# Performance work log

Measured on AMD Instinct MI355X. Metric: run time of the kernel, lower is better.

The kernel has to match this reference:

```python
import jax, jax.numpy as jnp
import numpy as np

EPS = 1e-5

def _ln(v, g, b):
    m = v.mean(-1, keepdims=True)
    var = ((v - m) ** 2).mean(-1, keepdims=True)
    return (v - m) * jax.lax.rsqrt(var + EPS) * g + b

def _causal_dwconv(x, w, b):
    # x: [B,S,C], w: [C,K] depthwise kernel, b: [C]; causal (left) padding
    K = w.shape[1]
    xt = x.transpose(0, 2, 1)  # [B,C,S]
    out = jax.lax.conv_general_dilated(xt, w[:, None, :], (1,), [(K - 1, 0)],
                                       dimension_numbers=('NCH', 'OIH', 'NCH'),
                                       feature_group_count=w.shape[0])
    return out.transpose(0, 2, 1) + b

def _ssm_scan(dt, Bm, Cm, x, A):
    # dt,x: [B,S,Di]; Bm,Cm: [B,S,N]; A: [Di,N] -> y: [B,S,Di]
    def step(h, inp):
        dt_t, B_t, C_t, x_t = inp
        dA = jnp.exp(dt_t[..., None] * A)                      # [B,Di,N]
        h = dA * h + dt_t[..., None] * B_t[:, None, :] * x_t[..., None]
        return h, jnp.einsum('bdn,bn->bd', h, C_t)
    h0 = jnp.zeros((dt.shape[0], A.shape[0], A.shape[1]), dt.dtype)
    xs = (dt.swapaxes(0, 1), Bm.swapaxes(0, 1), Cm.swapaxes(0, 1), x.swapaxes(0, 1))
    _, ys = jax.lax.scan(step, h0, xs)
    return ys.swapaxes(0, 1)

def _mamba_block(u, g, b, iW, cW, cB, xW, dW, dB, Al, Dpar, oW):
    # MambaBlock: LN -> Mamba -> residual
    Di, N = Al.shape
    R = dW.shape[1]
    xn = _ln(u, g, b)
    xz = xn @ iW.T                                  # [B,S,2*Di]
    xc, z = xz[..., :Di], xz[..., Di:]
    xc = jax.nn.silu(_causal_dwconv(xc, cW, cB))
    dbl = xc @ xW.T                                 # [B,S,R+2N]
    dt = jax.nn.softplus(dbl[..., :R] @ dW.T + dB)
    Bm, Cm = dbl[..., R:R + N], dbl[..., R + N:]
    A = -jnp.exp(Al)
    y = _ssm_scan(dt, Bm, Cm, xc, A) + xc * Dpar
    y = y * jax.nn.silu(z)
    return u + y @ oW.T

def _encoder(x, ln_g, ln_b, inW, convW, convB, xprojW, dtW, dtB, A_log, Dp, outW,
             ipW, ipB, opW, opB, fln_g, fln_b):
    L = ln_g.shape[0]
    h = x
    for i in range(L):
        xp = h @ ipW[i].T + ipB[i]
        Dh = xp.shape[-1] // 2
        yf = _mamba_block(xp[..., :Dh], ln_g[i, 0], ln_b[i, 0], inW[i, 0], convW[i, 0],
                          convB[i, 0], xprojW[i, 0], dtW[i, 0], dtB[i, 0], A_log[i, 0],
                          Dp[i, 0], outW[i, 0])
        xb_rev = jnp.flip(xp[..., Dh:], axis=1)
        yb = jnp.flip(_mamba_block(xb_rev, ln_g[i, 1], ln_b[i, 1], inW[i, 1], convW[i, 1],
                                   convB[i, 1], xprojW[i, 1], dtW[i, 1], dtB[i, 1],
                                   A_log[i, 1], Dp[i, 1], outW[i, 1]), axis=1)
        h = jnp.concatenate([yf, yb], axis=-1) @ opW[i].T + opB[i]
        # dropout is identity in eval mode
    return _ln(h, fln_g, fln_b)

def setup_inputs() -> dict:
    key = jax.random.key(0)
    L, B, S, D = 2, 2, 1024, 512
    Dh, Di, N, K, R = 256, 512, 16, 4, 16
    ks = jax.random.split(key, 9)
    s = 0.02
    x = jax.random.normal(ks[0], (B, S, D), jnp.float32)
    inW = jax.random.normal(ks[1], (L, 2, 2 * Di, Dh)) * s
    convW = jax.random.normal(ks[2], (L, 2, Di, K)) * 0.2
    xprojW = jax.random.normal(ks[3], (L, 2, R + 2 * N, Di)) * s
    dtW = jax.random.normal(ks[4], (L, 2, Di, R)) * (R ** -0.5)
    u = jax.random.uniform(ks[5], (L, 2, Di))
    dt = jnp.exp(u * (np.log(0.1) - np.log(0.001)) + np.log(0.001))
    dtB = dt + jnp.log(-jnp.expm1(-dt))          # inverse softplus init
    A_log = jnp.log(jnp.broadcast_to(jnp.arange(1, N + 1, dtype=jnp.float32), (L, 2, Di, N)))
    outW = jax.random.normal(ks[6], (L, 2, Dh, Di)) * s
    ipW = jax.random.normal(ks[7], (L, D, D)) * s
    opW = jax.random.normal(ks[8], (L, D, D)) * s
    return dict(x=x, ln_g=jnp.ones((L, 2, Dh)), ln_b=jnp.zeros((L, 2, Dh)), inW=inW,
                convW=convW, convB=jnp.zeros((L, 2, Di)), xprojW=xprojW, dtW=dtW, dtB=dtB,
                A_log=A_log, Dp=jnp.ones((L, 2, Di)), outW=outW, ipW=ipW,
                ipB=jnp.zeros((L, D)), opW=opW, opB=jnp.zeros((L, D)),
                fln_g=jnp.ones((D,)), fln_b=jnp.zeros((D,)))

def reference(x, ln_g, ln_b, inW, convW, convB, xprojW, dtW, dtB, A_log, Dp, outW,
              ipW, ipB, opW, opB, fln_g, fln_b):
    return _encoder(x, ln_g, ln_b, inW, convW, convB, xprojW, dtW, dtB, A_log, Dp, outW,
                    ipW, ipB, opW, opB, fln_g, fln_b)
```

## Files before the change

### kernel.cpp

```cpp
#include <hip/hip_runtime.h>
#include <hip/hip_bf16.h>
#include <math.h>

typedef __hip_bfloat16 bf16;
typedef __attribute__((ext_vector_type(8))) short s8v;
typedef __attribute__((ext_vector_type(4))) float f4v;

#define B_ 2
#define S_ 1024
#define D_ 512
#define DH_ 256
#define DI_ 512
#define N_ 16
#define R_ 16
#define M_ 2048
#define M2_ 4096
#define T_ 16
#define CN_ 64
#define NC_ 576

#define IPW_N (2*512*512)
#define INW_N (4*1024*256)
#define OUTW_N (4*256*512)
#define OPW_N (2*512*512)

__global__ __launch_bounds__(256) void k_castall(
    const float* __restrict__ ipW, const float* __restrict__ inW,
    const float* __restrict__ outW, const float* __restrict__ opW,
    bf16* __restrict__ ipWb, bf16* __restrict__ inWb,
    bf16* __restrict__ outWb, bf16* __restrict__ opWb) {
  int i = (blockIdx.x * 256 + threadIdx.x) * 4;
  const float* s; bf16* dst; int off;
  if (i < IPW_N)                  { s = ipW;  dst = ipWb;  off = i; }
  else if (i < IPW_N + INW_N)     { s = inW;  dst = inWb;  off = i - IPW_N; }
  else if (i < IPW_N + INW_N + OUTW_N) { s = outW; dst = outWb; off = i - IPW_N - INW_N; }
  else if (i < IPW_N + INW_N + OUTW_N + OPW_N)
                                  { s = opW;  dst = opWb;  off = i - IPW_N - INW_N - OUTW_N; }
  else return;
  float4 v = *(const float4*)&s[off];
  dst[off + 0] = __float2bfloat16(v.x);
  dst[off + 1] = __float2bfloat16(v.y);
  dst[off + 2] = __float2bfloat16(v.z);
  dst[off + 3] = __float2bfloat16(v.w);
}

__global__ __launch_bounds__(256) void k_castv(const float* __restrict__ src,
                                               bf16* __restrict__ dst, int n) {
  int i = (blockIdx.x * 256 + threadIdx.x) * 4;
  if (i >= n) return;
  float4 v = *(const float4*)&src[i];
  dst[i + 0] = __float2bfloat16(v.x);
  dst[i + 1] = __float2bfloat16(v.y);
  dst[i + 2] = __float2bfloat16(v.z);
  dst[i + 3] = __float2bfloat16(v.w);
}

__global__ __launch_bounds__(256) void k_prep(const float* __restrict__ dtW,
                                              const float* __restrict__ xprojW,
                                              bf16* __restrict__ Wcomb) {
  int idx = blockIdx.x * 256 + threadIdx.x;
  if (idx >= 4 * NC_ * 512) return;
  int k = idx & 511;
  int row = (idx >> 9) % NC_;
  int wi = idx / (NC_ * 512);
  float v = 0.f;
  if (row < 512) {
    const float* dw = dtW + (size_t)wi * 512 * 16 + row * 16;
    const float* xw = xprojW + (size_t)wi * 48 * 512;
#pragma unroll
    for (int r = 0; r < 16; r++) v += dw[r] * xw[r * 512 + k];
  } else if (row < 544) {
    v = xprojW[(size_t)wi * 48 * 512 + (16 + row - 512) * 512 + k];
  }
  Wcomb[idx] = __float2bfloat16(v);
}

__global__ __launch_bounds__(256) void k_mgemm(
    const bf16* __restrict__ A, const float* __restrict__ Af,
    const bf16* __restrict__ W, long Wstr,
    const float* __restrict__ bias, int bstr,
    const float* res,
    float* C, bf16* Cb, int ldc, int K, int ep) {
  __shared__ short As[64][40];
  __shared__ short Ws[64][40];
  const int bm = blockIdx.y * 64, bn = blockIdx.x * 64;
  const int seg = bm >> 11;
  const bf16* Wp = W + (size_t)seg * Wstr;
  const float* bp = bias ? bias + (size_t)seg * bstr : nullptr;
  const int tid = threadIdx.x;
  const int wave = tid >> 6, lane = tid & 63;
  const int q = lane >> 4, l15 = lane & 15;
  const int trow = tid >> 2, tcol = (tid & 3) * 8;

  f4v acc[4];
#pragma unroll
  for (int s = 0; s < 4; s++) acc[s] = (f4v){0.f, 0.f, 0.f, 0.f};

  for (int k0 = 0; k0 < K; k0 += 32) {
    if (ep == 4) {
      int ck = k0 + tcol;
      const float* src = (ck < 256)
          ? Af + (size_t)(bm + trow) * 256 + ck
          : Af + (size_t)M_ * 256 + (size_t)((bm + trow) ^ 1023) * 256 + (ck - 256);
      float4 f0 = *(const float4*)src;
      float4 f1 = *(const float4*)(src + 4);
      float fv[8] = {f0.x, f0.y, f0.z, f0.w, f1.x, f1.y, f1.z, f1.w};
      short tmp[8];
#pragma unroll
      for (int i = 0; i < 8; i++) {
        bf16 b = __float2bfloat16(fv[i]);
        tmp[i] = *(short*)&b;
      }
      *(uint4*)&As[trow][tcol] = *(uint4*)tmp;
    } else {
      *(uint4*)&As[trow][tcol] = *(const uint4*)&A[(size_t)(bm + trow) * K + k0 + tcol];
    }
    *(uint4*)&Ws[trow][tcol] = *(const uint4*)&Wp[(size_t)(bn + trow) * K + k0 + tcol];
    __syncthreads();
    s8v bfrag = *(const s8v*)&Ws[wave * 16 + l15][q * 8];
#pragma unroll
    for (int s = 0; s < 4; s++) {
      s8v afrag = *(const s8v*)&As[s * 16 + l15][q * 8];
      acc[s] = __builtin_amdgcn_mfma_f32_16x16x32_bf16(afrag, bfrag, acc[s], 0, 0, 0);
    }
    __syncthreads();
  }
  const int col = bn + wave * 16 + l15;
#pragma unroll
  for (int s = 0; s < 4; s++) {
#pragma unroll
    for (int r = 0; r < 4; r++) {
      int row = bm + s * 16 + q * 4 + r;
      float v = acc[s][r];
      if (ep == 0) {
        if (bp) v += bp[col];
        if (res) v += res[(size_t)row * ldc + col];
        C[(size_t)row * ldc + col] = v;
      } else if (ep == 2) {
        if (col < 512) {
          v += bp[col];
          v = (v > 20.f) ? v : log1pf(expf(v));
        }
        C[(size_t)row * ldc + col] = v;
      } else if (ep == 3) {
        v += bp[col];
        if (col < 256)
          C[(size_t)row * 256 + col] = v;
        else
          C[(size_t)M_ * 256 + (size_t)(row ^ 1023) * 256 + (col - 256)] = v;
      } else {
        v += bp[col];
        C[(size_t)row * 512 + col] = v;
        Cb[(size_t)row * 512 + col] = __float2bfloat16(v);
      }
    }
  }
}

__global__ __launch_bounds__(256) void k_ln(const float* __restrict__ X,
                                            const float* __restrict__ g,
                                            const float* __restrict__ bta,
                                            int gstr, void* __restrict__ Y,
                                            int C, int out_bf16) {
  const int row = blockIdx.x;
  const int sel = (row >= M_) ? gstr : 0;
  const float* xr = X + (size_t)row * C;
  const int tid = threadIdx.x;
  const int per = C >> 8;
  float vals[2];
  float sum = 0.f, sumsq = 0.f;
  for (int i = 0; i < per; i++) {
    float v = xr[tid + i * 256];
    vals[i] = v;
    sum += v;
    sumsq += v * v;
  }
#pragma unroll
  for (int off = 1; off < 64; off <<= 1) {
    sum += __shfl_xor(sum, off, 64);
    sumsq += __shfl_xor(sumsq, off, 64);
  }
  __shared__ float s1[4], s2[4];
  int wid = tid >> 6, lane = tid & 63;
  if (lane == 0) { s1[wid] = sum; s2[wid] = sumsq; }
  __syncthreads();
  if (tid == 0) {
    float a = 0.f, c2 = 0.f;
    for (int w = 0; w < 4; w++) { a += s1[w]; c2 += s2[w]; }
    s1[0] = a; s2[0] = c2;
  }
  __syncthreads();
  float mean = s1[0] / (float)C;
  float var = s2[0] / (float)C - mean * mean;
  float rstd = rsqrtf(var + 1e-5f);
  for (int i = 0; i < per; i++) {
    int c = tid + i * 256;
    float y = (vals[i] - mean) * rstd * g[sel + c] + bta[sel + c];
    if (out_bf16)
      ((bf16*)Y)[(size_t)row * C + c] = __float2bfloat16(y);
    else
      ((float*)Y)[(size_t)row * C + c] = y;
  }
}

__global__ __launch_bounds__(256) void k_conv(const float* __restrict__ xz,
                                              const float* __restrict__ convW,
                                              const float* __restrict__ convB,
                                              bf16* __restrict__ outb) {
  int idx = blockIdx.x * 256 + threadIdx.x;
  if (idx >= M2_ * DI_) return;
  int d = idx & (DI_ - 1);
  int row = idx >> 9;
  int seg = row >> 11;
  int t = row & (S_ - 1);
  const float* w = convW + seg * DI_ * 4;
  float acc = convB[seg * DI_ + d];
#pragma unroll
  for (int k = 0; k < 4; k++) {
    int dt_ = k - 3;
    if (t + dt_ >= 0)
      acc += w[d * 4 + k] * xz[(size_t)(row + dt_) * 1024 + d];
  }
  float s = acc / (1.f + __expf(-acc));
  outb[idx] = __float2bfloat16(s);
}

__global__ __launch_bounds__(256) void k_scanA(
    const float* __restrict__ dtbc,
    const bf16* __restrict__ xcb,
    const float* __restrict__ A_log,
    float* __restrict__ P,
    float* __restrict__ hend) {
  const int blk = blockIdx.x;
  const int half = blk & 1;
  const int c = (blk >> 1) & (CN_ - 1);
  const int s = blk >> 7;
  const int dir = s >> 1;
  const int d = half * 256 + threadIdx.x;
  const int r0 = s * S_ + c * T_;
  __shared__ float Bs[T_][16];
  for (int i = threadIdx.x; i < T_ * 16; i += 256) {
    int t = i >> 4, n = i & 15;
    Bs[t][n] = dtbc[(size_t)(r0 + t) * NC_ + 512 + n];
  }
  float Av[16];
#pragma unroll
  for (int n = 0; n < 16; n++) Av[n] = -__expf(A_log[dir * DI_ * 16 + d * 16 + n]);
  float dtv[T_], xv[T_];
#pragma unroll
  for (int t = 0; t < T_; t++) {
    size_t row = (size_t)(r0 + t);
    dtv[t] = dtbc[row * NC_ + d];
    xv[t]  = __bfloat162float(xcb[row * 512 + d]);
  }
  __syncthreads();
  float h[16], Pr[16];
#pragma unroll
  for (int n = 0; n < 16; n++) { h[n] = 0.f; Pr[n] = 1.f; }
#pragma unroll
  for (int t = 0; t < T_; t++) {
    float dtx = dtv[t] * xv[t];
#pragma unroll
    for (int n = 0; n < 16; n++) {
      float a = __expf(dtv[t] * Av[n]);
      h[n] = a * h[n] + dtx * Bs[t][n];
      Pr[n] *= a;
    }
  }
  size_t base = (((size_t)s * CN_ + c) * 16) * 512 + d;
#pragma unroll
  for (int n = 0; n < 16; n++) {
    P[base + (size_t)n * 512] = Pr[n];
    hend[base + (size_t)n * 512] = h[n];
  }
}

__global__ __launch_bounds__(256) void k_scanB(
    const float* __restrict__ P,
    const float* __restrict__ hend,
    float* __restrict__ Hinit) {
  int idx = blockIdx.x * 256 + threadIdx.x;
  if (idx >= 4 * 16 * 512) return;
  int d = idx & 511;
  int n = (idx >> 9) & 15;
  int s = idx >> 13;
  float H = 0.f;
  for (int c = 0; c < CN_; c++) {
    size_t o = (((size_t)s * CN_ + c) * 16 + n) * 512 + d;
    float p = P[o];
    float he = hend[o];
    Hinit[o] = H;
    H = p * H + he;
  }
}

__global__ __launch_bounds__(256) void k_scanC(
    const float* __restrict__ dtbc,
    const float* __restrict__ xz,
    const bf16* __restrict__ xcb,
    const float* __restrict__ A_log,
    const float* __restrict__ Dp,
    const float* __restrict__ Hinit,
    bf16* __restrict__ ybf) {
  const int blk = blockIdx.x;
  const int half = blk & 1;
  const int c = (blk >> 1) & (CN_ - 1);
  const int s = blk >> 7;
  const int dir = s >> 1;
  const int d = half * 256 + threadIdx.x;
  const int r0 = s * S_ + c * T_;
  __shared__ float Bs[T_][16], Cs[T_][16];
  for (int i = threadIdx.x; i < T_ * 16; i += 256) {
    int t = i >> 4, n = i & 15;
    size_t ro = (size_t)(r0 + t) * NC_;
    Bs[t][n] = dtbc[ro + 512 + n];
    Cs[t][n] = dtbc[ro + 528 + n];
  }
  float Av[16];
#pragma unroll
  for (int n = 0; n < 16; n++) Av[n] = -__expf(A_log[dir * DI_ * 16 + d * 16 + n]);
  float Dd = Dp[dir * DI_ + d];
  float dtv[T_], xv[T_], zv[T_];
#pragma unroll
  for (int t = 0; t < T_; t++) {
    size_t row = (size_t)(r0 + t);
    dtv[t] = dtbc[row * NC_ + d];
    xv[t]  = __bfloat162float(xcb[row * 512 + d]);
    zv[t]  = xz[row * 1024 + 512 + d];
  }
  float h[16];
  size_t hbase = (((size_t)s * CN_ + c) * 16) * 512 + d;
#pragma unroll
  for (int n = 0; n < 16; n++) h[n] = Hinit[hbase + (size_t)n * 512];
  __syncthreads();
#pragma unroll
  for (int t = 0; t < T_; t++) {
    float dtx = dtv[t] * xv[t];
    float acc = 0.f;
#pragma unroll
    for (int n = 0; n < 16; n++) {
      float a = __expf(dtv[t] * Av[n]);
      h[n] = a * h[n] + dtx * Bs[t][n];
      acc += h[n] * Cs[t][n];
    }
    float sil = zv[t] / (1.f + __expf(-zv[t]));
    ybf[(size_t)(r0 + t) * 512 + d] =
        __float2bfloat16((acc + xv[t] * Dd) * sil);
  }
}

extern "C" void kernel_launch(void* const* d_in, const int* in_sizes, int n_in,
                              void* d_out, int out_size, void* d_ws, size_t ws_size,
                              hipStream_t stream) {
  const float* x     = (const float*)d_in[0];
  const float* ln_g  = (const float*)d_in[1];
  const float* ln_b  = (const float*)d_in[2];
  const float* inW   = (const float*)d_in[3];
  const float* convW = (const float*)d_in[4];
  const float* convB = (const float*)d_in[5];
  const float* xprojW= (const float*)d_in[6];
  const float* dtW   = (const float*)d_in[7];
  const float* dtB   = (const float*)d_in[8];
  const float* A_log = (const float*)d_in[9];
  const float* Dp    = (const float*)d_in[10];
  const float* outW  = (const float*)d_in[11];
  const float* ipW   = (const float*)d_in[12];
  const float* ipB   = (const float*)d_in[13];
  const float* opW   = (const float*)d_in[14];
  const float* opB   = (const float*)d_in[15];
  const float* fln_g = (const float*)d_in[16];
  const float* fln_b = (const float*)d_in[17];
  float* out = (float*)d_out;

  float* w = (float*)d_ws;
  float* xz2   = w;  w += (size_t)M2_ * 1024;
  float* h_cur = w;  w += (size_t)M_ * D_;
  float* u_f   = w;  w += (size_t)M2_ * DH_;
  float* dtbc2 = w;  w += (size_t)M2_ * NC_;
  float* Pbuf  = w;  w += (size_t)4 * CN_ * 16 * 512;
  float* hend  = w;  w += (size_t)4 * CN_ * 16 * 512;
  float* Hinit = Pbuf;
  bf16* bw = (bf16*)w;
  bf16* xb    = bw;  bw += (size_t)M_ * D_;
  bf16* xnb2  = bw;  bw += (size_t)M2_ * DH_;
  bf16* xcvb2 = bw;  bw += (size_t)M2_ * DI_;
  bf16* ybf2  = bw;  bw += (size_t)M2_ * DI_;
  bf16* ipWb  = bw;  bw += (size_t)IPW_N;
  bf16* inWb  = bw;  bw += (size_t)INW_N;
  bf16* outWb = bw;  bw += (size_t)OUTW_N;
  bf16* opWb  = bw;  bw += (size_t)OPW_N;
  bf16* Wcomb = bw;  bw += (size_t)4 * NC_ * 512;

  int tot = IPW_N + INW_N + OUTW_N + OPW_N;
  k_castall<<<(tot / 4 + 255) / 256, 256, 0, stream>>>(
      ipW, inW, outW, opW, ipWb, inWb, outWb, opWb);
  k_prep<<<(4 * NC_ * 512 + 255) / 256, 256, 0, stream>>>(dtW, xprojW, Wcomb);
  k_castv<<<(M_ * D_ / 4 + 255) / 256, 256, 0, stream>>>(x, xb, M_ * D_);

  for (int li = 0; li < 2; li++) {
    k_mgemm<<<dim3(8, 32), 256, 0, stream>>>(
        xb, nullptr, ipWb + (size_t)li * D_ * D_, 0,
        ipB + (size_t)li * D_, 0, nullptr, u_f, nullptr, 256, D_, 3);
    k_ln<<<M2_, 256, 0, stream>>>(u_f, ln_g + li * 2 * DH_, ln_b + li * 2 * DH_,
                                  DH_, (void*)xnb2, DH_, 1);
    k_mgemm<<<dim3(16, 64), 256, 0, stream>>>(
        xnb2, nullptr, inWb + (size_t)li * 2 * 1024 * DH_, (long)1024 * DH_,
        nullptr, 0, nullptr, xz2, nullptr, 1024, DH_, 0);
    k_conv<<<(M2_ * DI_ + 255) / 256, 256, 0, stream>>>(
        xz2, convW + li * 2 * DI_ * 4, convB + li * 2 * DI_, xcvb2);
    k_mgemm<<<dim3(9, 64), 256, 0, stream>>>(
        xcvb2, nullptr, Wcomb + (size_t)li * 2 * NC_ * 512, (long)NC_ * 512,
        dtB + li * 2 * DI_, DI_, nullptr, dtbc2, nullptr, NC_, 512, 2);
    k_scanA<<<4 * CN_ * 2, 256, 0, stream>>>(
        dtbc2, xcvb2, A_log + (size_t)li * 2 * DI_ * N_, Pbuf, hend);
    k_scanB<<<(4 * 16 * 512 + 255) / 256, 256, 0, stream>>>(Pbuf, hend, Hinit);
    k_scanC<<<4 * CN_ * 2, 256, 0, stream>>>(
        dtbc2, xz2, xcvb2, A_log + (size_t)li * 2 * DI_ * N_,
        Dp + (size_t)li * 2 * DI_, Hinit, ybf2);
    k_mgemm<<<dim3(4, 64), 256, 0, stream>>>(
        ybf2, nullptr, outWb + (size_t)li * 2 * DH_ * DI_, (long)DH_ * DI_,
        nullptr, 0, u_f, u_f, nullptr, 256, DI_, 0);
    k_mgemm<<<dim3(8, 32), 256, 0, stream>>>(
        nullptr, u_f, opWb + (size_t)li * D_ * D_, 0,
        opB + (size_t)li * D_, 0, nullptr, h_cur, xb, 512, D_, 4);
  }
  k_ln<<<M_, 256, 0, stream>>>(h_cur, fln_g, fln_b, 0, (void*)out, D_, 0);
}
```

Measured before the change: 385.8 us.

## Merge prep kernels, add 128x128 GEMM, store xz in bf16, lengthen scan chunks

New measurement: 465.3 us. +20.6%, slower.

```diff
diff --git a/kernel.cpp b/kernel.cpp
--- a/kernel.cpp
+++ b/kernel.cpp
@@ -12,67 +12,135 @@
 #define DH_ 256
 #define DI_ 512
 #define N_ 16
-#define R_ 16
 #define M_ 2048
 #define M2_ 4096
-#define T_ 16
-#define CN_ 64
-#define NC_ 576
+#define T_ 32
+#define CN_ 32
+#define NC_ 640
 
 #define IPW_N (2*512*512)
 #define INW_N (4*1024*256)
 #define OUTW_N (4*256*512)
 #define OPW_N (2*512*512)
-
-__global__ __launch_bounds__(256) void k_castall(
+#define PREP_R0 ((IPW_N+INW_N+OUTW_N+OPW_N)/4)
+#define PREP_R1 (4*NC_*512)
+#define PREP_R2 ((M_*D_)/4)
+
+__global__ __launch_bounds__(256) void k_prep_all(
     const float* __restrict__ ipW, const float* __restrict__ inW,
     const float* __restrict__ outW, const float* __restrict__ opW,
+    const float* __restrict__ dtW, const float* __restrict__ xprojW,
+    const float* __restrict__ x,
     bf16* __restrict__ ipWb, bf16* __restrict__ inWb,
-    bf16* __restrict__ outWb, bf16* __restrict__ opWb) {
-  int i = (blockIdx.x * 256 + threadIdx.x) * 4;
-  const float* s; bf16* dst; int off;
-  if (i < IPW_N)                  { s = ipW;  dst = ipWb;  off = i; }
-  else if (i < IPW_N + INW_N)     { s = inW;  dst = inWb;  off = i - IPW_N; }
-  else if (i < IPW_N + INW_N + OUTW_N) { s = outW; dst = outWb; off = i - IPW_N - INW_N; }
-  else if (i < IPW_N + INW_N + OUTW_N + OPW_N)
-                                  { s = opW;  dst = opWb;  off = i - IPW_N - INW_N - OUTW_N; }
-  else return;
-  float4 v = *(const float4*)&s[off];
-  dst[off + 0] = __float2bfloat16(v.x);
-  dst[off + 1] = __float2bfloat16(v.y);
-  dst[off + 2] = __float2bfloat16(v.z);
-  dst[off + 3] = __float2bfloat16(v.w);
-}
-
-__global__ __launch_bounds__(256) void k_castv(const float* __restrict__ src,
-                                               bf16* __restrict__ dst, int n) {
-  int i = (blockIdx.x * 256 + threadIdx.x) * 4;
-  if (i >= n) return;
-  float4 v = *(const float4*)&src[i];
-  dst[i + 0] = __float2bfloat16(v.x);
-  dst[i + 1] = __float2bfloat16(v.y);
-  dst[i + 2] = __float2bfloat16(v.z);
-  dst[i + 3] = __float2bfloat16(v.w);
-}
-
-__global__ __launch_bounds__(256) void k_prep(const float* __restrict__ dtW,
-                                              const float* __restrict__ xprojW,
-                                              bf16* __restrict__ Wcomb) {
-  int idx = blockIdx.x * 256 + threadIdx.x;
-  if (idx >= 4 * NC_ * 512) return;
-  int k = idx & 511;
-  int row = (idx >> 9) % NC_;
-  int wi = idx / (NC_ * 512);
-  float v = 0.f;
-  if (row < 512) {
-    const float* dw = dtW + (size_t)wi * 512 * 16 + row * 16;
-    const float* xw = xprojW + (size_t)wi * 48 * 512;
-#pragma unroll
-    for (int r = 0; r < 16; r++) v += dw[r] * xw[r * 512 + k];
-  } else if (row < 544) {
-    v = xprojW[(size_t)wi * 48 * 512 + (16 + row - 512) * 512 + k];
-  }
-  Wcomb[idx] = __float2bfloat16(v);
+    bf16* __restrict__ outWb, bf16* __restrict__ opWb,
+    bf16* __restrict__ Wcomb, bf16* __restrict__ xb) {
+  int i = blockIdx.x * 256 + threadIdx.x;
+  if (i < PREP_R0) {
+    int e = i * 4;
+    const float* s; bf16* dst; int off;
+    if (e < IPW_N)                       { s = ipW;  dst = ipWb;  off = e; }
+    else if (e < IPW_N + INW_N)          { s = inW;  dst = inWb;  off = e - IPW_N; }
+    else if (e < IPW_N + INW_N + OUTW_N) { s = outW; dst = outWb; off = e - IPW_N - INW_N; }
+    else                                 { s = opW;  dst = opWb;  off = e - IPW_N - INW_N - OUTW_N; }
+    float4 v = *(const float4*)&s[off];
+    dst[off + 0] = __float2bfloat16(v.x);
+    dst[off + 1] = __float2bfloat16(v.y);
+    dst[off + 2] = __float2bfloat16(v.z);
+    dst[off + 3] = __float2bfloat16(v.w);
+  } else if (i < PREP_R0 + PREP_R1) {
+    int idx = i - PREP_R0;
+    int k = idx & 511;
+    int row = (idx >> 9) % NC_;
+    int wi = idx / (NC_ * 512);
+    float v = 0.f;
+    if (row < 512) {
+      const float* dw = dtW + (size_t)wi * 512 * 16 + row * 16;
+      const float* xw = xprojW + (size_t)wi * 48 * 512;
+#pragma unroll
+      for (int r = 0; r < 16; r++) v += dw[r] * xw[r * 512 + k];
+    } else if (row < 544) {
+      v = xprojW[(size_t)wi * 48 * 512 + (16 + row - 512) * 512 + k];
+    }
+    Wcomb[idx] = __float2bfloat16(v);
+  } else if (i < PREP_R0 + PREP_R1 + PREP_R2) {
+    int e = (i - PREP_R0 - PREP_R1) * 4;
+    float4 v = *(const float4*)&x[e];
+    xb[e + 0] = __float2bfloat16(v.x);
+    xb[e + 1] = __float2bfloat16(v.y);
+    xb[e + 2] = __float2bfloat16(v.z);
+    xb[e + 3] = __float2bfloat16(v.w);
+  }
+}
+
+__global__ __launch_bounds__(256) void k_mg128(
+    const bf16* __restrict__ A, const bf16* __restrict__ W, long Wstr,
+    const float* __restrict__ bias, int bstr,
+    float* __restrict__ C, bf16* __restrict__ Cb, int ldc, int K, int ep) {
+  __shared__ short As[128][40];
+  __shared__ short Ws[128][40];
+  const int bm = blockIdx.y * 128, bn = blockIdx.x * 128;
+  const int seg = bm >> 11;
+  const bf16* Wp = W + (size_t)seg * Wstr;
+  const float* bp = bias ? bias + (size_t)seg * bstr : nullptr;
+  const int tid = threadIdx.x;
+  const int wave = tid >> 6, lane = tid & 63;
+  const int wr = (wave >> 1) * 64, wc = (wave & 1) * 64;
+  const int q = lane >> 4, l15 = lane & 15;
+  const int sr = tid >> 1;
+  const int sc = (tid & 1) * 16;
+
+  f4v acc[4][4];
+#pragma unroll
+  for (int i = 0; i < 4; i++)
+#pragma unroll
+    for (int j = 0; j < 4; j++) acc[i][j] = (f4v){0.f, 0.f, 0.f, 0.f};
+
+  for (int k0 = 0; k0 < K; k0 += 32) {
+    const bf16* Ap = A + (size_t)(bm + sr) * K + k0 + sc;
+    const bf16* Wq = Wp + (size_t)(bn + sr) * K + k0 + sc;
+    uint4 a0 = *(const uint4*)Ap;
+    uint4 a1 = *(const uint4*)(Ap + 8);
+    uint4 w0 = *(const uint4*)Wq;
+    uint4 w1 = *(const uint4*)(Wq + 8);
+    *(uint4*)&As[sr][sc] = a0;
+    *(uint4*)&As[sr][sc + 8] = a1;
+    *(uint4*)&Ws[sr][sc] = w0;
+    *(uint4*)&Ws[sr][sc + 8] = w1;
+    __syncthreads();
+    s8v af[4], bf[4];
+#pragma unroll
+    for (int i = 0; i < 4; i++) {
+      af[i] = *(const s8v*)&As[wr + i * 16 + l15][q * 8];
+      bf[i] = *(const s8v*)&Ws[wc + i * 16 + l15][q * 8];
+    }
+#pragma unroll
+    for (int i = 0; i < 4; i++)
+#pragma unroll
+      for (int j = 0; j < 4; j++)
+        acc[i][j] = __builtin_amdgcn_mfma_f32_16x16x32_bf16(af[i], bf[j], acc[i][j], 0, 0, 0);
+    __syncthreads();
+  }
+#pragma unroll
+  for (int i = 0; i < 4; i++) {
+#pragma unroll
+    for (int j = 0; j < 4; j++) {
+      int col = bn + wc + j * 16 + l15;
+#pragma unroll
+      for (int r = 0; r < 4; r++) {
+        int row = bm + wr + i * 16 + q * 4 + r;
+        float v = acc[i][j][r];
+        if (ep == 1) {
+          Cb[(size_t)row * ldc + col] = __float2bfloat16(v);
+        } else {
+          if (col < 512) {
+            v += bp[col];
+            v = (v > 20.f) ? v : log1pf(expf(v));
+          }
+          C[(size_t)row * ldc + col] = v;
+        }
+      }
+    }
+  }
 }
 
 __global__ __launch_bounds__(256) void k_mgemm(
@@ -135,12 +203,6 @@
       if (ep == 0) {
         if (bp) v += bp[col];
         if (res) v += res[(size_t)row * ldc + col];
-        C[(size_t)row * ldc + col] = v;
-      } else if (ep == 2) {
-        if (col < 512) {
-          v += bp[col];
-          v = (v > 20.f) ? v : log1pf(expf(v));
-        }
         C[(size_t)row * ldc + col] = v;
       } else if (ep == 3) {
         v += bp[col];
@@ -203,7 +265,7 @@
   }
 }
 
-__global__ __launch_bounds__(256) void k_conv(const float* __restrict__ xz,
+__global__ __launch_bounds__(256) void k_conv(const bf16* __restrict__ xz,
                                               const float* __restrict__ convW,
                                               const float* __restrict__ convB,
                                               bf16* __restrict__ outb) {
@@ -219,7 +281,7 @@
   for (int k = 0; k < 4; k++) {
     int dt_ = k - 3;
     if (t + dt_ >= 0)
-      acc += w[d * 4 + k] * xz[(size_t)(row + dt_) * 1024 + d];
+      acc += w[d * 4 + k] * __bfloat162float(xz[(size_t)(row + dt_) * 1024 + d]);
   }
   float s = acc / (1.f + __expf(-acc));
   outb[idx] = __float2bfloat16(s);
@@ -234,7 +296,7 @@
   const int blk = blockIdx.x;
   const int half = blk & 1;
   const int c = (blk >> 1) & (CN_ - 1);
-  const int s = blk >> 7;
+  const int s = blk >> 6;
   const int dir = s >> 1;
   const int d = half * 256 + threadIdx.x;
   const int r0 = s * S_ + c * T_;
@@ -246,23 +308,18 @@
   float Av[16];
 #pragma unroll
   for (int n = 0; n < 16; n++) Av[n] = -__expf(A_log[dir * DI_ * 16 + d * 16 + n]);
-  float dtv[T_], xv[T_];
-#pragma unroll
+  __syncthreads();
+  float h[16], Pr[16];
+#pragma unroll
+  for (int n = 0; n < 16; n++) { h[n] = 0.f; Pr[n] = 1.f; }
   for (int t = 0; t < T_; t++) {
     size_t row = (size_t)(r0 + t);
-    dtv[t] = dtbc[row * NC_ + d];
-    xv[t]  = __bfloat162float(xcb[row * 512 + d]);
-  }
-  __syncthreads();
-  float h[16], Pr[16];
-#pragma unroll
-  for (int n = 0; n < 16; n++) { h[n] = 0.f; Pr[n] = 1.f; }
-#pragma unroll
-  for (int t = 0; t < T_; t++) {
-    float dtx = dtv[t] * xv[t];
+    float dtv = dtbc[row * NC_ + d];
+    float xv = __bfloat162float(xcb[row * 512 + d]);
+    float dtx = dtv * xv;
 #pragma unroll
     for (int n = 0; n < 16; n++) {
-      float a = __expf(dtv[t] * Av[n]);
+      float a = __expf(dtv * Av[n]);
       h[n] = a * h[n] + dtx * Bs[t][n];
       Pr[n] *= a;
     }
@@ -296,7 +353,7 @@
 
 __global__ __launch_bounds__(256) void k_scanC(
     const float* __restrict__ dtbc,
-    const float* __restrict__ xz,
+    const bf16* __restrict__ xz,
     const bf16* __restrict__ xcb,
     const float* __restrict__ A_log,
     const float* __restrict__ Dp,
@@ -305,7 +362,7 @@
   const int blk = blockIdx.x;
   const int half = blk & 1;
   const int c = (blk >> 1) & (CN_ - 1);
-  const int s = blk >> 7;
+  const int s = blk >> 6;
   const int dir = s >> 1;
   const int d = half * 256 + threadIdx.x;
   const int r0 = s * S_ + c * T_;
@@ -320,32 +377,26 @@
 #pragma unroll
   for (int n = 0; n < 16; n++) Av[n] = -__expf(A_log[dir * DI_ * 16 + d * 16 + n]);
   float Dd = Dp[dir * DI_ + d];
-  float dtv[T_], xv[T_], zv[T_];
-#pragma unroll
+  float h[16];
+  size_t hbase = (((size_t)s * CN_ + c) * 16) * 512 + d;
+#pragma unroll
+  for (int n = 0; n < 16; n++) h[n] = Hinit[hbase + (size_t)n * 512];
+  __syncthreads();
   for (int t = 0; t < T_; t++) {
     size_t row = (size_t)(r0 + t);
-    dtv[t] = dtbc[row * NC_ + d];
-    xv[t]  = __bfloat162float(xcb[row * 512 + d]);
-    zv[t]  = xz[row * 1024 + 512 + d];
-  }
-  float h[16];
-  size_t hbase = (((size_t)s * CN_ + c) * 16) * 512 + d;
-#pragma unroll
-  for (int n = 0; n < 16; n++) h[n] = Hinit[hbase + (size_t)n * 512];
-  __syncthreads();
-#pragma unroll
-  for (int t = 0; t < T_; t++) {
-    float dtx = dtv[t] * xv[t];
+    float dtv = dtbc[row * NC_ + d];
+    float xv = __bfloat162float(xcb[row * 512 + d]);
+    float zv = __bfloat162float(xz[row * 1024 + 512 + d]);
+    float dtx = dtv * xv;
     float acc = 0.f;
 #pragma unroll
     for (int n = 0; n < 16; n++) {
-      float a = __expf(dtv[t] * Av[n]);
+      float a = __expf(dtv * Av[n]);
       h[n] = a * h[n] + dtx * Bs[t][n];
       acc += h[n] * Cs[t][n];
     }
-    float sil = zv[t] / (1.f + __expf(-zv[t]));
-    ybf[(size_t)(r0 + t) * 512 + d] =
-        __float2bfloat16((acc + xv[t] * Dd) * sil);
+    float sil = zv / (1.f + __expf(-zv));
+    ybf[row * 512 + d] = __float2bfloat16((acc + xv * Dd) * sil);
   }
 }
 
@@ -373,7 +424,6 @@
   float* out = (float*)d_out;
 
   float* w = (float*)d_ws;
-  float* xz2   = w;  w += (size_t)M2_ * 1024;
   float* h_cur = w;  w += (size_t)M_ * D_;
   float* u_f   = w;  w += (size_t)M2_ * DH_;
   float* dtbc2 = w;  w += (size_t)M2_ * NC_;
@@ -381,6 +431,7 @@
   float* hend  = w;  w += (size_t)4 * CN_ * 16 * 512;
   float* Hinit = Pbuf;
   bf16* bw = (bf16*)w;
+  bf16* xz2b  = bw;  bw += (size_t)M2_ * 1024;
   bf16* xb    = bw;  bw += (size_t)M_ * D_;
   bf16* xnb2  = bw;  bw += (size_t)M2_ * DH_;
   bf16* xcvb2 = bw;  bw += (size_t)M2_ * DI_;
@@ -391,11 +442,10 @@
   bf16* opWb  = bw;  bw += (size_t)OPW_N;
   bf16* Wcomb = bw;  bw += (size_t)4 * NC_ * 512;
 
-  int tot = IPW_N + INW_N + OUTW_N + OPW_N;
-  k_castall<<<(tot / 4 + 255) / 256, 256, 0, stream>>>(
-      ipW, inW, outW, opW, ipWb, inWb, outWb, opWb);
-  k_prep<<<(4 * NC_ * 512 + 255) / 256, 256, 0, stream>>>(dtW, xprojW, Wcomb);
-  k_castv<<<(M_ * D_ / 4 + 255) / 256, 256, 0, stream>>>(x, xb, M_ * D_);
+  int prep_threads = PREP_R0 + PREP_R1 + PREP_R2;
+  k_prep_all<<<(prep_threads + 255) / 256, 256, 0, stream>>>(
+      ipW, inW, outW, opW, dtW, xprojW, x,
+      ipWb, inWb, outWb, opWb, Wcomb, xb);
 
   for (int li = 0; li < 2; li++) {
     k_mgemm<<<dim3(8, 32), 256, 0, stream>>>(
@@ -403,19 +453,19 @@
         ipB + (size_t)li * D_, 0, nullptr, u_f, nullptr, 256, D_, 3);
     k_ln<<<M2_, 256, 0, stream>>>(u_f, ln_g + li * 2 * DH_, ln_b + li * 2 * DH_,
                                   DH_, (void*)xnb2, DH_, 1);
-    k_mgemm<<<dim3(16, 64), 256, 0, stream>>>(
-        xnb2, nullptr, inWb + (size_t)li * 2 * 1024 * DH_, (long)1024 * DH_,
-        nullptr, 0, nullptr, xz2, nullptr, 1024, DH_, 0);
+    k_mg128<<<dim3(8, 32), 256, 0, stream>>>(
+        xnb2, inWb + (size_t)li * 2 * 1024 * DH_, (long)1024 * DH_,
+        nullptr, 0, nullptr, xz2b, 1024, DH_, 1);
     k_conv<<<(M2_ * DI_ + 255) / 256, 256, 0, stream>>>(
-        xz2, convW + li * 2 * DI_ * 4, convB + li * 2 * DI_, xcvb2);
-    k_mgemm<<<dim3(9, 64), 256, 0, stream>>>(
-        xcvb2, nullptr, Wcomb + (size_t)li * 2 * NC_ * 512, (long)NC_ * 512,
-        dtB + li * 2 * DI_, DI_, nullptr, dtbc2, nullptr, NC_, 512, 2);
+        xz2b, convW + li * 2 * DI_ * 4, convB + li * 2 * DI_, xcvb2);
+    k_mg128<<<dim3(NC_ / 128, 32), 256, 0, stream>>>(
+        xcvb2, Wcomb + (size_t)li * 2 * NC_ * 512, (long)NC_ * 512,
+        dtB + li * 2 * DI_, DI_, dtbc2, nullptr, NC_, 512, 2);
     k_scanA<<<4 * CN_ * 2, 256, 0, stream>>>(
         dtbc2, xcvb2, A_log + (size_t)li * 2 * DI_ * N_, Pbuf, hend);
     k_scanB<<<(4 * 16 * 512 + 255) / 256, 256, 0, stream>>>(Pbuf, hend, Hinit);
     k_scanC<<<4 * CN_ * 2, 256, 0, stream>>>(
-        dtbc2, xz2, xcvb2, A_log + (size_t)li * 2 * DI_ * N_,
+        dtbc2, xz2b, xcvb2, A_log + (size_t)li * 2 * DI_ * N_,
         Dp + (size_t)li * 2 * DI_, Hinit, ybf2);
     k_mgemm<<<dim3(4, 64), 256, 0, stream>>>(
         ybf2, nullptr, outWb + (size_t)li * 2 * DH_ * DI_, (long)DH_ * DI_,
```
